# Kernel tuning notes

Measured on AMD Instinct MI355X. Metric: run time of the kernel, lower is better.

## Reference

```python
import jax, jax.numpy as jnp
import numpy as np

NUM_HEADS = 8
HEAD_DIM = 64
HIDDEN_SIZE = 128
TOP_K = 16
EPS = 1e-6


def setup_inputs() -> dict:
    key = jax.random.key(0)
    k1, k2, k3 = jax.random.split(key, 3)
    B, H, S, D = 4, NUM_HEADS, 1024, HEAD_DIM
    return {
        "keys": jax.random.normal(k1, (B, H, S, D), dtype=jnp.float32),
        "values": jax.random.normal(k2, (B, H, S, D), dtype=jnp.float32),
        "queries": jax.random.normal(k3, (B, H, S, D), dtype=jnp.float32),
    }


def _project(x):
    # replicate [B,H,S,D] along last dim to cover HIDDEN_SIZE basis indices
    D = x.shape[-1]
    if D >= HIDDEN_SIZE:
        return x[..., :HIDDEN_SIZE]
    repeats = (HIDDEN_SIZE + D - 1) // D
    return jnp.tile(x, (1, 1, 1, repeats))[..., :HIDDEN_SIZE]


def reference(keys, values, queries):
    B, H, S, D = keys.shape
    b_idx = jnp.arange(B)[:, None, None]   # [B,1,1]
    h_idx = jnp.arange(H)[None, :, None]   # [1,H,1]

    # ---- update: scatter-add outer products into assigned memory bank ----
    assignments = jnp.argmax(jnp.abs(_project(keys)), axis=-1)  # [B,H,S]
    outer = values[..., :, None] * keys[..., None, :]           # [B,H,S,D,D] (v k^T)
    M = jnp.zeros((B, H, HIDDEN_SIZE, D, D), dtype=keys.dtype)
    M = M.at[b_idx, h_idx, assignments].add(outer)
    z = jnp.zeros((B, H, HIDDEN_SIZE, D), dtype=keys.dtype)
    z = z.at[b_idx, h_idx, assignments].add(keys)

    # ---- retrieve: top-k basis selection, gather-matvec, weighted combine ----
    scores = jnp.abs(_project(queries))                          # [B,H,S,HIDDEN]
    top_scores, top_idx = jax.lax.top_k(scores, TOP_K)           # [B,H,S,K]
    weights = jax.nn.softmax(top_scores, axis=-1)

    output = jnp.zeros((B, H, S, D), dtype=queries.dtype)
    for k in range(TOP_K):
        mem = top_idx[..., k]                                    # [B,H,S]
        M_sel = M[b_idx, h_idx, mem]                             # [B,H,S,D,D]
        z_sel = z[b_idx, h_idx, mem]                             # [B,H,S,D]
        num = jnp.einsum('bhsde,bhse->bhsd', M_sel, queries)
        den = jnp.einsum('bhsd,bhsd->bhs', z_sel, queries)[..., None] + EPS
        output = output + weights[..., k:k + 1] * (num / den)
    return output
```

## Files before the change

### kernel.cpp

```cpp
#include <hip/hip_runtime.h>
#include <math.h>

#define S_LEN 1024
#define EPS 1e-6f

typedef __attribute__((ext_vector_type(8)))  short bf16x8;
typedef __attribute__((ext_vector_type(4)))  short bf16x4;
typedef __attribute__((ext_vector_type(16))) float float16v;


__device__ __forceinline__ void bar_lgkm() {
    asm volatile("s_waitcnt lgkmcnt(0)" ::: "memory");
    __builtin_amdgcn_s_barrier();
    __builtin_amdgcn_sched_barrier(0);
    asm volatile("" ::: "memory");
}

#define PIN(x) asm volatile("" : "+v"(x))

__device__ __forceinline__ unsigned short f2bf(float f) {
    unsigned int u = __float_as_uint(f);
    unsigned int r = (u + 0x7fffu + ((u >> 16) & 1u)) >> 16;
    return (unsigned short)r;
}

__device__ __forceinline__ bf16x8 pack8(float4 a, float4 b) {
    bf16x8 r;
    r[0] = (short)f2bf(a.x); r[1] = (short)f2bf(a.y);
    r[2] = (short)f2bf(a.z); r[3] = (short)f2bf(a.w);
    r[4] = (short)f2bf(b.x); r[5] = (short)f2bf(b.y);
    r[6] = (short)f2bf(b.z); r[7] = (short)f2bf(b.w);
    return r;
}

__global__ __launch_bounds__(512) void k_pre(const float* __restrict__ keys,
                                             const float* __restrict__ queries,
                                             int* __restrict__ kcnt2,
                                             unsigned short* __restrict__ klist2,
                                             int* __restrict__ qcnt2,
                                             unsigned* __restrict__ qpair,
                                             unsigned char* __restrict__ qflag,
                                             float* __restrict__ out) {
    const int bh   = blockIdx.x >> 5;
    const int blk  = blockIdx.x & 31;
    const int wv   = threadIdx.x >> 6;
    const int lane = threadIdx.x & 63;

    __shared__ int khist[64], qhist[64];
    __shared__ alignas(16) unsigned rq_s[8][4][64];
    if (threadIdx.x < 64) { khist[threadIdx.x] = 0; qhist[threadIdx.x] = 0; }
    __syncthreads();

    const int s0 = blk * 32 + wv * 4;
    float kv[4], qv[4];
    #pragma unroll
    for (int i = 0; i < 4; ++i) {
        kv[i] = keys   [((size_t)bh * 1024 + s0 + i) * 64 + lane];
        qv[i] = queries[((size_t)bh * 1024 + s0 + i) * 64 + lane];
    }

    {
        float4 zz = {0.f, 0.f, 0.f, 0.f};
        float4* po = (float4*)(out + (size_t)blockIdx.x * 2048);
        po[threadIdx.x] = zz;
    }

    #pragma unroll
    for (int i = 0; i < 4; ++i) { PIN(kv[i]); PIN(qv[i]); }

    unsigned ud[4];
    #pragma unroll
    for (int i = 0; i < 4; ++i) {
        ud[i] = __float_as_uint(qv[i]) & 0x7fffffffu;
        rq_s[wv][i][lane] = ud[i];
    }

    float bv[4]; int bi[4];
    #pragma unroll
    for (int i = 0; i < 4; ++i) { bv[i] = fabsf(kv[i]); bi[i] = lane; }
    #pragma unroll
    for (int off = 1; off < 64; off <<= 1) {
        #pragma unroll
        for (int i = 0; i < 4; ++i) {
            float ov = __shfl_xor(bv[i], off, 64);
            int   oi = __shfl_xor(bi[i], off, 64);
            if (ov > bv[i] || (ov == bv[i] && oi < bi[i])) { bv[i] = ov; bi[i] = oi; }
        }
    }
    #pragma unroll
    for (int i = 0; i < 4; ++i) {
        if (lane == 0) {
            int pos = atomicAdd(&khist[bi[i]], 1);
            klist2[((size_t)bh * 64 + bi[i]) * 1024 + blk * 32 + pos] =
                (unsigned short)(s0 + i);
        }
    }

    int gt[4] = {0, 0, 0, 0};
    #pragma unroll
    for (int k4 = 0; k4 < 16; ++k4) {
        #pragma unroll
        for (int i = 0; i < 4; ++i) {
            const uint4 vv = *(const uint4*)&rq_s[wv][i][k4 * 4];
            gt[i] += (vv.x > ud[i]) ? 1 : 0;
            gt[i] += (vv.y > ud[i]) ? 1 : 0;
            gt[i] += (vv.z > ud[i]) ? 1 : 0;
            gt[i] += (vv.w > ud[i]) ? 1 : 0;
        }
    }
    int S[4];
    #pragma unroll
    for (int i = 0; i < 4; ++i) S[i] = gt[i];
    #pragma unroll
    for (int off = 1; off < 64; off <<= 1) {
        #pragma unroll
        for (int i = 0; i < 4; ++i) S[i] += __shfl_xor(S[i], off, 64);
    }
    float e[4];
    #pragma unroll
    for (int i = 0; i < 4; ++i) e[i] = expf(__uint_as_float(ud[i]));
    int copies[4], contrib[4], rank[4];
    #pragma unroll
    for (int i = 0; i < 4; ++i) {
        if (S[i] == 2016) {
            contrib[i] = (gt[i] < 8);
            copies[i]  = contrib[i] ? 2 : 0;
            rank[i]    = gt[i];
        } else {
            int eq = 0, eql = 0;
            #pragma unroll
            for (int k = 0; k < 64; ++k) {
                unsigned ui = (unsigned)__builtin_amdgcn_readlane((int)ud[i], k);
                eq  += (ui == ud[i]) ? 1 : 0;
                eql += (ui == ud[i] && k < lane) ? 1 : 0;
            }
            int pos_low  = 2 * gt[i] + eql;
            int pos_high = pos_low + eq;
            copies[i]  = (pos_low < 16 ? 1 : 0) + (pos_high < 16 ? 1 : 0);
            contrib[i] = (pos_low < 16);
            rank[i]    = 15;
        }
    }
    float ce[4];
    #pragma unroll
    for (int i = 0; i < 4; ++i) ce[i] = (float)copies[i] * e[i];
    #pragma unroll
    for (int off = 1; off < 64; off <<= 1) {
        #pragma unroll
        for (int i = 0; i < 4; ++i) ce[i] += __shfl_xor(ce[i], off, 64);
    }
    #pragma unroll
    for (int i = 0; i < 4; ++i) {
        if (contrib[i]) {
            int pos = atomicAdd(&qhist[lane], 1);
            unsigned wb = __float_as_uint(e[i] / ce[i]) & 0xFFFFC000u;
            qpair[((size_t)bh * 64 + lane) * 1024 + blk * 32 + pos] =
                wb | ((unsigned)rank[i] << 10) | (unsigned)(s0 + i);
        }
        if (qflag && lane == 0)
            qflag[bh * 1024 + s0 + i] = (S[i] == 2016) ? 0 : 1;
    }
    __syncthreads();
    if (threadIdx.x < 64) {
        kcnt2[(bh * 64 + threadIdx.x) * 32 + blk] = khist[threadIdx.x];
        qcnt2[(bh * 64 + threadIdx.x) * 32 + blk] = qhist[threadIdx.x];
    }
}

template <bool SC>
__global__ __launch_bounds__(256) void k_mainB(const float* __restrict__ keys,
                                               const float* __restrict__ values,
                                               const float* __restrict__ queries,
                                               const int* __restrict__ kcnt2,
                                               const unsigned short* __restrict__ klist2,
                                               const int* __restrict__ qcnt2,
                                               const unsigned* __restrict__ qpair,
                                               unsigned short* __restrict__ Obuf,
                                               float* __restrict__ out) {
    const int g     = blockIdx.x;
    const int bh    = g >> 6;
    const int bank  = g & 63;
    const int t     = threadIdx.x;
    const int lane  = t & 63;
    const int grp   = t >> 6;

    __shared__ alignas(16) unsigned short M_bf[64 * 64];
    __shared__ alignas(16) unsigned short Q_bf[64 * 64];
    __shared__ alignas(16) unsigned short Ou_bf[64 * 68];
    __shared__ unsigned short s_match[256];
    __shared__ unsigned q_ent[256];
    __shared__ int    koffs_s[33], qoffs_s[33];
    __shared__ float  z_s[64];
    __shared__ double den_s[64];
    __shared__ float  w_s[2][64];
    __shared__ int    sq_s[2][64];

    if (t < 64) {
        int i = t & 31;
        int c = (t < 32) ? kcnt2[(bh * 64 + bank) * 32 + i]
                         : qcnt2[(bh * 64 + bank) * 32 + i];
        #pragma unroll
        for (int off = 1; off < 32; off <<= 1) {
            int o = __shfl(c, t - off, 64);
            if (i >= off) c += o;
        }
        if (t < 32) { if (i == 0) koffs_s[0] = 0; koffs_s[i + 1] = c; }
        else        { if (i == 0) qoffs_s[0] = 0; qoffs_s[i + 1] = c; }
    }
    bar_lgkm();

    const int nq = qoffs_s[32];
    const int nm = koffs_s[32];
    if (nq == 0) return;
    const size_t listbase = (size_t)(bh * 64 + bank) * 1024;
    if (nm == 0) {
        if constexpr (SC) {
            for (int jg = t; jg < nq; jg += 256) {
                int seg = 0;
                #pragma unroll
                for (int i = 1; i < 32; ++i) if (jg >= qoffs_s[i]) seg = i;
                unsigned e = qpair[listbase + seg * 32 + (jg - qoffs_s[seg])];
                int r = (e >> 10) & 15;
                if (r < 8) {
                    uint4 z4 = {0u, 0u, 0u, 0u};
                    uint4* dst = (uint4*)&Obuf[(((size_t)bh * 1024 +
                                 (e & 1023u)) * 8 + r) * 64];
                    #pragma unroll
                    for (int x = 0; x < 8; ++x) dst[x] = z4;
                }
            }
        }
        return;
    }

    {
        if (t < min(256, nm)) {
            int seg = 0;
            #pragma unroll
            for (int i = 1; i < 32; ++i) if (t >= koffs_s[i]) seg = i;
            s_match[t] = klist2[listbase + seg * 32 + (t - koffs_s[seg])];
        }
        if (t < min(256, nq)) {
            int seg = 0;
            #pragma unroll
            for (int i = 1; i < 32; ++i) if (t >= qoffs_s[i]) seg = i;
            q_ent[t] = qpair[listbase + seg * 32 + (t - qoffs_s[seg])];
        }
    }
    bar_lgkm();

    {
        float* kstf = (float*)Q_bf;
        float* vstf = (float*)Ou_bf;
        float acc[16];
        #pragma unroll
        for (int m = 0; m < 16; ++m) acc[m] = 0.f;
        float zacc = 0.f;
        const float* kb = keys   + (size_t)bh * S_LEN * 64;
        const float* vb = values + (size_t)bh * S_LEN * 64;
        int win = 0;
        for (int cb = 0; cb < nm; cb += 32) {
            const int cn = min(32, nm - cb);
            if ((cb & ~255) != win) {
                bar_lgkm();
                win = cb & ~255;
                int wn = min(256, nm - win);
                if (t < wn) {
                    int idx = win + t, seg = 0;
                    #pragma unroll
                    for (int i = 1; i < 32; ++i) if (idx >= koffs_s[i]) seg = i;
                    s_match[t] = klist2[listbase + seg * 32 + (idx - koffs_s[seg])];
                }
                bar_lgkm();
            }
            if (cb > 0) bar_lgkm();
            {
                int r = t >> 3, c8 = t & 7;
                if (r < cn) {
                    int s = s_match[(cb - win) + r];
                    const float4* ks = (const float4*)(kb + (size_t)s * 64 + c8 * 8);
                    float4 k0 = ks[0], k1 = ks[1];
                    const float4* vs = (const float4*)(vb + (size_t)s * 64 + c8 * 8);
                    float4 w0 = vs[0], w1 = vs[1];
                    float4* kd = (float4*)&kstf[r * 64 + c8 * 8];
                    kd[0] = k0; kd[1] = k1;
                    float4* vd = (float4*)&vstf[r * 64 + c8 * 8];
                    vd[0] = w0; vd[1] = w1;
                }
            }
            bar_lgkm();
            for (int r = 0; r < cn; ++r) {
                float kv = kstf[r * 64 + lane];
                #pragma unroll
                for (int m = 0; m < 16; ++m)
                    acc[m] += vstf[r * 64 + grp * 16 + m] * kv;
            }
            if (t < 64)
                for (int r = 0; r < cn; ++r) zacc += kstf[r * 64 + t];
        }
        #pragma unroll
        for (int m = 0; m < 16; ++m) {
            int dv = grp * 16 + m;
            M_bf[dv * 64 + (((lane >> 3) ^ (dv & 7)) << 3) + (lane & 7)] = f2bf(acc[m]);
        }
        if (t < 64) z_s[t] = zacc;
    }
    bar_lgkm();

    const float* qb = queries + (size_t)bh * S_LEN * 64;
    float*       ob = out     + (size_t)bh * S_LEN * 64;
    unsigned short* obuf_b = SC ? Obuf + (size_t)bh * 1024 * 512 : nullptr;
    const int dvh = grp >> 1, jh = grp & 1;
    const int hi  = lane >> 5;
    const int jq  = t >> 2, cq = t & 3;

    int prev_nb = 0;
    bool have_pf = false;
    float4 f0, f1, f2, f3;
    unsigned pe = 0;
    for (int qloc = 0, batch = 0; qloc < nq; qloc += 64, ++batch) {
        const int nb  = min(64, nq - qloc);
        const int cur = batch & 1;

        if (qloc != 0 && (qloc & 255) == 0) {
            if (qloc + t < nq) {
                int jg = qloc + t;
                int seg = 0;
                #pragma unroll
                for (int i = 1; i < 32; ++i) if (jg >= qoffs_s[i]) seg = i;
                q_ent[t] = qpair[listbase + seg * 32 + (jg - qoffs_s[seg])];
            }
            bar_lgkm();
        }

        unsigned e = 0;
        const bool act = (jq < nb);
        if (act) {
            e = have_pf ? pe : q_ent[(qloc & 255) + jq];
            if (!have_pf) {
                const float4* src =
                    (const float4*)(qb + (size_t)(e & 1023u) * 64 + cq * 16);
                f0 = src[0]; f1 = src[1]; f2 = src[2]; f3 = src[3];
            }
        }

        if (batch > 0) {
            #pragma unroll
            for (int jj = 0; jj < 16; ++jj) {
                int j = grp * 16 + jj;
                if (j < prev_nb) {
                    unsigned short vb16 = Ou_bf[j * 68 + lane];
                    int sr = sq_s[1 - cur][j];
                    int s  = sr & 1023;
                    if constexpr (SC) {
                        int r = (sr >> 10) & 15;
                        if (r < 8)
                            obuf_b[((size_t)s * 8 + r) * 64 + lane] = vb16;
                        else
                            unsafeAtomicAdd(&ob[(size_t)s * 64 + lane],
                                __uint_as_float((unsigned)vb16 << 16));
                    } else {
                        unsafeAtomicAdd(&ob[(size_t)s * 64 + lane],
                            __uint_as_float((unsigned)vb16 << 16));
                    }
                }
            }
        }

        {
            bf16x8 p0 = {}, p1 = {};
            double d = 0.0;
            if (act) {
                if ((t & 3) == 0) {
                    sq_s[cur][jq] = (int)(e & 0x3FFFu);
                    w_s[cur][jq]  = __uint_as_float(e & 0xFFFFC000u);
                }
                p0 = pack8(f0, f1);
                p1 = pack8(f2, f3);
                const float4* zz4 = (const float4*)&z_s[cq * 16];
                float4 z0 = zz4[0], z1 = zz4[1], z2 = zz4[2], z3 = zz4[3];
                double da, db;
                da  = (double)z0.x * f0.x + (double)z0.y * f0.y + (double)z0.z * f0.z + (double)z0.w * f0.w;
                db  = (double)z1.x * f1.x + (double)z1.y * f1.y + (double)z1.z * f1.z + (double)z1.w * f1.w;
                da += (double)z2.x * f2.x + (double)z2.y * f2.y + (double)z2.z * f2.z + (double)z2.w * f2.w;
                db += (double)z3.x * f3.x + (double)z3.y * f3.y + (double)z3.z * f3.z + (double)z3.w * f3.w;
                d = da + db;
            }
            int c0 = cq * 2;
            *(bf16x8*)&Q_bf[jq * 64 + ((c0 ^ (jq & 7)) << 3)]       = p0;
            *(bf16x8*)&Q_bf[jq * 64 + (((c0 + 1) ^ (jq & 7)) << 3)] = p1;
            d += __shfl_xor(d, 1, 64);
            d += __shfl_xor(d, 2, 64);
            if ((t & 3) == 0) den_s[jq] = d;
        }

        {
            const int qn = qloc + 64;
            have_pf = false;
            if (qn < nq && (qn & 255) != 0) {
                int nbn = min(64, nq - qn);
                if (jq < nbn) {
                    pe = q_ent[(qn & 255) + jq];
                    const float4* src =
                        (const float4*)(qb + (size_t)(pe & 1023u) * 64 + cq * 16);
                    f0 = src[0]; f1 = src[1]; f2 = src[2]; f3 = src[3];
                    have_pf = true;
                }
            }
        }
        bar_lgkm();

        float16v C;
        #pragma unroll
        for (int i = 0; i < 16; ++i) C[i] = 0.f;
        const int am = dvh * 32 + (lane & 31);
        const int bn = jh  * 32 + (lane & 31);
        #pragma unroll
        for (int ks = 0; ks < 4; ++ks) {
            int ch = ks * 2 + hi;
            bf16x8 af = *(const bf16x8*)&M_bf[am * 64 + ((ch ^ (am & 7)) << 3)];
            bf16x8 bf = *(const bf16x8*)&Q_bf[bn * 64 + ((ch ^ (bn & 7)) << 3)];
            C = __builtin_amdgcn_mfma_f32_32x32x16_bf16(af, bf, C, 0, 0, 0);
        }
        {
            double den = den_s[bn];
            float  w   = w_s[cur][bn];
            float rinv = (float)((double)w / (den + (double)EPS));
            #pragma unroll
            for (int rq = 0; rq < 4; ++rq) {
                bf16x4 pk;
                pk[0] = (short)f2bf(C[rq * 4 + 0] * rinv);
                pk[1] = (short)f2bf(C[rq * 4 + 1] * rinv);
                pk[2] = (short)f2bf(C[rq * 4 + 2] * rinv);
                pk[3] = (short)f2bf(C[rq * 4 + 3] * rinv);
                *(bf16x4*)&Ou_bf[bn * 68 + dvh * 32 + rq * 8 + hi * 4] = pk;
            }
        }
        bar_lgkm();
        prev_nb = nb;
    }
    {
        const int cur = (((nq + 63) >> 6) - 1) & 1;
        #pragma unroll
        for (int jj = 0; jj < 16; ++jj) {
            int j = grp * 16 + jj;
            if (j < prev_nb) {
                unsigned short vb16 = Ou_bf[j * 68 + lane];
                int sr = sq_s[cur][j];
                int s  = sr & 1023;
                if constexpr (SC) {
                    int r = (sr >> 10) & 15;
                    if (r < 8)
                        obuf_b[((size_t)s * 8 + r) * 64 + lane] = vb16;
                    else
                        unsafeAtomicAdd(&ob[(size_t)s * 64 + lane],
                            __uint_as_float((unsigned)vb16 << 16));
                } else {
                    unsafeAtomicAdd(&ob[(size_t)s * 64 + lane],
                        __uint_as_float((unsigned)vb16 << 16));
                }
            }
        }
    }
}

__global__ __launch_bounds__(256) void k_reduce(const unsigned short* __restrict__ Obuf,
                                                const unsigned char* __restrict__ qflag,
                                                float* __restrict__ out) {
    const int wv   = threadIdx.x >> 6;
    const int lane = threadIdx.x & 63;
    const int q0   = (blockIdx.x * 4 + wv) * 8;
    #pragma unroll
    for (int i = 0; i < 8; ++i) {
        int q = q0 + i;
        if (qflag[q]) continue;
        const unsigned short* obr = Obuf + (size_t)q * 512;
        float acc = 0.f;
        #pragma unroll
        for (int r = 0; r < 8; ++r)
            acc += __uint_as_float((unsigned)obr[r * 64 + lane] << 16);
        out[(size_t)q * 64 + lane] = acc;
    }
}

extern "C" void kernel_launch(void* const* d_in, const int* in_sizes, int n_in,
                              void* d_out, int out_size, void* d_ws, size_t ws_size,
                              hipStream_t stream) {
    const float* keys    = (const float*)d_in[0];
    const float* values  = (const float*)d_in[1];
    const float* queries = (const float*)d_in[2];
    char* ws = (char*)d_ws;
    int*            kcnt2  = (int*)(ws);
    int*            qcnt2  = (int*)(ws + 262144);
    unsigned short* klist2 = (unsigned short*)(ws + 524288);
    unsigned*       qpair  = (unsigned*)(ws + 4718592);
    unsigned char*  qflag  = (unsigned char*)(ws + 30416896);
    unsigned short* Obuf   = (unsigned short*)(ws + 30449664);
    const bool big2 = (ws_size >= 64004096u);

    k_pre<<<1024, 512, 0, stream>>>(keys, queries, kcnt2, klist2, qcnt2, qpair,
                                    big2 ? qflag : nullptr, (float*)d_out);
    if (big2) {
        k_mainB<true><<<2048, 256, 0, stream>>>(keys, values, queries, kcnt2,
                                                klist2, qcnt2, qpair, Obuf,
                                                (float*)d_out);
        k_reduce<<<1024, 256, 0, stream>>>(Obuf, qflag, (float*)d_out);
    } else {
        k_mainB<false><<<2048, 256, 0, stream>>>(keys, values, queries, kcnt2,
                                                 klist2, qcnt2, qpair, Obuf,
                                                 (float*)d_out);
    }
}
```

Measured before the change: 129.9 us.

## Split each bank's query list across two blocks to double grid parallelism

Each (batch-head, bank) workgroup is now split into two blocks, and each block handles half of that bank's query list. The grid grows from 2048 to 4096 blocks. The aim is better load balance and occupancy across CUs, since banks with long query lists serialize work in one block. The cost is that both blocks rebuild the same memory matrix M from the key/value lists, which doubles that accumulation work and its key/value reads.

```diff
diff --git a/kernel.cpp b/kernel.cpp
--- a/kernel.cpp
+++ b/kernel.cpp
@@ -178,8 +178,10 @@
                                                unsigned short* __restrict__ Obuf,
                                                float* __restrict__ out) {
     const int g     = blockIdx.x;
-    const int bh    = g >> 6;
-    const int bank  = g & 63;
+    const int gb    = g >> 1;
+    const int split = g & 1;
+    const int bh    = gb >> 6;
+    const int bank  = gb & 63;
     const int t     = threadIdx.x;
     const int lane  = t & 63;
     const int grp   = t >> 6;
@@ -211,11 +213,15 @@
 
     const int nq = qoffs_s[32];
     const int nm = koffs_s[32];
-    if (nq == 0) return;
+    const int half = (nq + 1) >> 1;
+    const int jlo  = split * half;
+    const int jhi  = min(nq, jlo + half);
+    const int nqL  = jhi - jlo;
+    if (nqL <= 0) return;
     const size_t listbase = (size_t)(bh * 64 + bank) * 1024;
     if (nm == 0) {
         if constexpr (SC) {
-            for (int jg = t; jg < nq; jg += 256) {
+            for (int jg = jlo + t; jg < jhi; jg += 256) {
                 int seg = 0;
                 #pragma unroll
                 for (int i = 1; i < 32; ++i) if (jg >= qoffs_s[i]) seg = i;
@@ -240,11 +246,12 @@
             for (int i = 1; i < 32; ++i) if (t >= koffs_s[i]) seg = i;
             s_match[t] = klist2[listbase + seg * 32 + (t - koffs_s[seg])];
         }
-        if (t < min(256, nq)) {
+        if (t < 256 && t < nqL) {
+            int jg = jlo + t;
             int seg = 0;
             #pragma unroll
-            for (int i = 1; i < 32; ++i) if (t >= qoffs_s[i]) seg = i;
-            q_ent[t] = qpair[listbase + seg * 32 + (t - qoffs_s[seg])];
+            for (int i = 1; i < 32; ++i) if (jg >= qoffs_s[i]) seg = i;
+            q_ent[t] = qpair[listbase + seg * 32 + (jg - qoffs_s[seg])];
         }
     }
     bar_lgkm();
@@ -318,13 +325,13 @@
     bool have_pf = false;
     float4 f0, f1, f2, f3;
     unsigned pe = 0;
-    for (int qloc = 0, batch = 0; qloc < nq; qloc += 64, ++batch) {
-        const int nb  = min(64, nq - qloc);
+    for (int qloc = 0, batch = 0; qloc < nqL; qloc += 64, ++batch) {
+        const int nb  = min(64, nqL - qloc);
         const int cur = batch & 1;
 
         if (qloc != 0 && (qloc & 255) == 0) {
-            if (qloc + t < nq) {
-                int jg = qloc + t;
+            if (qloc + t < nqL) {
+                int jg = jlo + qloc + t;
                 int seg = 0;
                 #pragma unroll
                 for (int i = 1; i < 32; ++i) if (jg >= qoffs_s[i]) seg = i;
@@ -397,8 +404,8 @@
         {
             const int qn = qloc + 64;
             have_pf = false;
-            if (qn < nq && (qn & 255) != 0) {
-                int nbn = min(64, nq - qn);
+            if (qn < nqL && (qn & 255) != 0) {
+                int nbn = min(64, nqL - qn);
                 if (jq < nbn) {
                     pe = q_ent[(qn & 255) + jq];
                     const float4* src =
@@ -440,7 +447,7 @@
         prev_nb = nb;
     }
     {
-        const int cur = (((nq + 63) >> 6) - 1) & 1;
+        const int cur = (((nqL + 63) >> 6) - 1) & 1;
         #pragma unroll
         for (int jj = 0; jj < 16; ++jj) {
             int j = grp * 16 + jj;
@@ -501,12 +508,12 @@
     k_pre<<<1024, 512, 0, stream>>>(keys, queries, kcnt2, klist2, qcnt2, qpair,
                                     big2 ? qflag : nullptr, (float*)d_out);
     if (big2) {
-        k_mainB<true><<<2048, 256, 0, stream>>>(keys, values, queries, kcnt2,
+        k_mainB<true><<<4096, 256, 0, stream>>>(keys, values, queries, kcnt2,
                                                 klist2, qcnt2, qpair, Obuf,
                                                 (float*)d_out);
         k_reduce<<<1024, 256, 0, stream>>>(Obuf, qflag, (float*)d_out);
     } else {
-        k_mainB<false><<<2048, 256, 0, stream>>>(keys, values, queries, kcnt2,
+        k_mainB<false><<<4096, 256, 0, stream>>>(keys, values, queries, kcnt2,
                                                  klist2, qcnt2, qpair, Obuf,
                                                  (float*)d_out);
     }
```

Result: slower. 149.7 us (+15.2%).
